# Kernel optimization log

Measured on AMD Instinct MI355X. Metric: run time of the kernel, lower is better.

## Reference

```python
import jax, jax.numpy as jnp
import numpy as np

WS = 8
NH = 6

def setup_inputs() -> dict:
    key = jax.random.key(0)
    ks = jax.random.split(key, 6)
    B, H, W, C = 4, 256, 256, 192
    return {
        "x": jax.random.normal(ks[0], (B, H * W, C), dtype=jnp.float32),
        "qkv_w": jax.random.normal(ks[1], (3 * C, C), dtype=jnp.float32) * 0.02,
        "qkv_b": jax.random.normal(ks[2], (3 * C,), dtype=jnp.float32) * 0.02,
        "proj_w": jax.random.normal(ks[3], (C, C), dtype=jnp.float32) * 0.02,
        "proj_b": jax.random.normal(ks[4], (C,), dtype=jnp.float32) * 0.02,
        "bias": jax.random.normal(ks[5], (NH, WS * WS, WS * WS), dtype=jnp.float32) * 0.02,
        "H": H,
        "W": W,
    }

def reference(x, qkv_w, qkv_b, proj_w, proj_b, bias, H, W):
    B, L, C = x.shape
    ws, nh = WS, NH
    hd = C // nh
    scale = hd ** -0.5
    H_pad = (H + ws - 1) // ws * ws
    W_pad = (W + ws - 1) // ws * ws
    pad_b, pad_r = H_pad - H, W_pad - W
    xv = x.reshape(B, H, W, C)
    if pad_b > 0 or pad_r > 0:
        xv = jnp.pad(xv, ((0, 0), (0, pad_b), (0, pad_r), (0, 0)))
    nHw, nWw = H_pad // ws, W_pad // ws
    # window partition: [B*nH*nW, ws*ws, C]
    xw = xv.reshape(B, nHw, ws, nWw, ws, C).transpose(0, 1, 3, 2, 4, 5)
    xw = xw.reshape(B * nHw * nWw, ws * ws, C)
    qkv = xw @ qkv_w.T + qkv_b  # [Bw, ws*ws, 3C]
    qkv = qkv.reshape(-1, ws * ws, 3, nh, hd).transpose(2, 0, 3, 1, 4)
    q, k, v = qkv[0], qkv[1], qkv[2]  # each [Bw, nh, ws*ws, hd]
    attn = jnp.einsum('bhqd,bhkd->bhqk', q * scale, k) + bias
    attn = jax.nn.softmax(attn, axis=-1)
    out = jnp.einsum('bhqk,bhkd->bhqd', attn, v)
    out = out.transpose(0, 2, 1, 3).reshape(-1, ws * ws, C)
    out = out @ proj_w.T + proj_b
    # window reverse: [B, H_pad, W_pad, C]
    out = out.reshape(B, nHw, nWw, ws, ws, C).transpose(0, 1, 3, 2, 4, 5)
    out = out.reshape(B, H_pad, W_pad, C)
    if pad_b > 0 or pad_r > 0:
        out = out[:, :H, :W, :]
    return out.reshape(B, H * W, C)
```

## Files before the change

kernel.cpp:

```cpp
#include <hip/hip_runtime.h>

typedef short bf16x8 __attribute__((ext_vector_type(8)));
typedef float f32x4 __attribute__((ext_vector_type(4)));

#define QKV_FRAG_SH 110592
#define PROJ_FRAG_SH 36864
#define BIAS2_OFF_B 294912
#define QKVB2_OFF_B 393216
#define SCALE 0.17677669529663689f
#define LOG2E 1.44269504088896341f
#define QSCALE (SCALE * LOG2E)
#define SMEM_BYTES 161792

__device__ __forceinline__ short f2bf(float f) {
  unsigned x = __float_as_uint(f);
  x = (x + 0x7FFFu + ((x >> 16) & 1u)) >> 16;
  return (short)x;
}

__global__ void cvt_w(const float* __restrict__ qkv_w,
                      const float* __restrict__ proj_w,
                      const float* __restrict__ bias,
                      const float* __restrict__ qkv_b,
                      short* __restrict__ wfrag,
                      float* __restrict__ bias2,
                      float* __restrict__ qkvb2) {
  int idx = blockIdx.x * 256 + threadIdx.x;
  if (idx < QKV_FRAG_SH) {
    int j = idx & 7, lane = (idx >> 3) & 63, t = idx >> 9;
    int nt = t / 6, ks = t - nt * 6;
    int n0 = nt * 16 + (lane & 15);
    float v = qkv_w[n0 * 192 + ks * 32 + (lane >> 4) * 8 + j];
    if (n0 < 192) v *= QSCALE;
    wfrag[idx] = f2bf(v);
  } else if (idx < QKV_FRAG_SH + PROJ_FRAG_SH) {
    int i2 = idx - QKV_FRAG_SH;
    int j = i2 & 7, lane = (i2 >> 3) & 63, t = i2 >> 9;
    int nt = t / 6, ks = t - nt * 6;
    wfrag[idx] = f2bf(proj_w[(nt * 16 + (lane & 15)) * 192 + ks * 32 + (lane >> 4) * 8 + j]);
  } else if (idx < QKV_FRAG_SH + PROJ_FRAG_SH + 24576) {
    int i3 = idx - (QKV_FRAG_SH + PROJ_FRAG_SH);
    int r = i3 & 3, nt = (i3 >> 2) & 3, lane = (i3 >> 4) & 63, mt = (i3 >> 10) & 3, h = i3 >> 12;
    int row = mt * 16 + (lane >> 4) * 4 + r;
    int col = nt * 16 + (lane & 15);
    bias2[i3] = bias[h * 4096 + row * 64 + col] * LOG2E;
  } else if (idx < QKV_FRAG_SH + PROJ_FRAG_SH + 24576 + 576) {
    int i4 = idx - (QKV_FRAG_SH + PROJ_FRAG_SH + 24576);
    qkvb2[i4] = qkv_b[i4] * (i4 < 192 ? QSCALE : 1.0f);
  }
}

__global__ __launch_bounds__(768, 3) void swin_fused(
    const float* __restrict__ x,
    const float* __restrict__ proj_b,
    const short* __restrict__ wfrag,
    const float* __restrict__ bias2,
    const float* __restrict__ qkvb2,
    float* __restrict__ out) {
  extern __shared__ short smem[];
  short* buf = smem;
  short* q_l = smem + 25600;
  short* k_l = smem + 39424;
  short* v_l = smem + 53248;
  short* p_s = smem + 67072;

  const short* wq = wfrag;
  const short* wp = wfrag + QKV_FRAG_SH;

  const int tid = threadIdx.x;
  const int w = tid >> 6, lane = tid & 63, quad = lane >> 4, lm = lane & 15;

  int goff[4], loff[4];
  #pragma unroll
  for (int i = 0; i < 4; ++i) {
    int idx4 = tid + i * 768;
    int chunk = idx4 / 384;
    int off = idx4 - chunk * 384;
    goff[i] = chunk * 49152 + off * 4;
    loff[i] = (chunk * 8 + off / 48) * 200 + (off % 48) * 4;
  }

  size_t base;
  {
    int wid = blockIdx.x;
    int b = wid >> 10, rem = wid & 1023, wh = rem >> 5, ww = rem & 31;
    base = ((size_t)b * 65536 + (size_t)(wh * 8) * 256 + (size_t)(ww * 8)) * 192;
    const float* xp = x + base;
    #pragma unroll
    for (int i = 0; i < 4; ++i) {
      float4 f = *(const float4*)(xp + goff[i]);
      short4 s = { f2bf(f.x), f2bf(f.y), f2bf(f.z), f2bf(f.w) };
      *(short4*)&buf[loff[i]] = s;
    }
  }
  __syncthreads();

  float4 pf[4];
  size_t nbase = 0;
  #pragma unroll 1
  for (int it = 0; it < 16; ++it) {
    const int cur = (it & 1) * 12800;
    const int nxt = 12800 - cur;

    if (it < 15) {
      int wid = (it + 1) * 256 + blockIdx.x;
      int b = wid >> 10, rem = wid & 1023, wh = rem >> 5, ww = rem & 31;
      nbase = ((size_t)b * 65536 + (size_t)(wh * 8) * 256 + (size_t)(ww * 8)) * 192;
      const float* xp = x + nbase;
      #pragma unroll
      for (int i = 0; i < 4; ++i) pf[i] = *(const float4*)(xp + goff[i]);
    }

    {
      const int nt0 = w * 3;
      f32x4 acc[3][4];
      #pragma unroll
      for (int j = 0; j < 3; ++j) {
        float bn = qkvb2[(nt0 + j) * 16 + lm];
        #pragma unroll
        for (int mm = 0; mm < 4; ++mm) acc[j][mm] = (f32x4){bn, bn, bn, bn};
      }
      #pragma unroll 2
      for (int ks = 0; ks < 6; ++ks) {
        bf16x8 a[4];
        #pragma unroll
        for (int mm = 0; mm < 4; ++mm)
          a[mm] = *(const bf16x8*)&buf[cur + (mm * 16 + lm) * 200 + ks * 32 + quad * 8];
        #pragma unroll
        for (int j = 0; j < 3; ++j) {
          bf16x8 bwf = *(const bf16x8*)&wq[((nt0 + j) * 6 + ks) * 512 + lane * 8];
          #pragma unroll
          for (int mm = 0; mm < 4; ++mm)
            acc[j][mm] = __builtin_amdgcn_mfma_f32_16x16x32_bf16(a[mm], bwf, acc[j][mm], 0, 0, 0);
        }
      }
      if (w < 4) {
        #pragma unroll
        for (int j = 0; j < 3; ++j) {
          int nt = nt0 + j, h = nt >> 1, dh = nt & 1;
          #pragma unroll
          for (int mm = 0; mm < 4; ++mm) {
            int rb = h * 64 + mm * 16 + quad * 4;
            #pragma unroll
            for (int r = 0; r < 4; ++r)
              q_l[(rb + r) * 36 + dh * 16 + lm] = f2bf(acc[j][mm][r]);
          }
        }
      } else if (w < 8) {
        #pragma unroll
        for (int j = 0; j < 3; ++j) {
          int nt = nt0 + j, h = (nt - 12) >> 1, dh = nt & 1;
          #pragma unroll
          for (int mm = 0; mm < 4; ++mm) {
            int rb = h * 64 + mm * 16 + quad * 4;
            #pragma unroll
            for (int r = 0; r < 4; ++r)
              k_l[(rb + r) * 36 + dh * 16 + lm] = f2bf(acc[j][mm][r]);
          }
        }
      } else {
        #pragma unroll
        for (int j = 0; j < 3; ++j) {
          int nt = nt0 + j, h = (nt - 24) >> 1, dh = nt & 1;
          #pragma unroll
          for (int mm = 0; mm < 4; ++mm) {
            short4 s4 = { f2bf(acc[j][mm][0]), f2bf(acc[j][mm][1]),
                          f2bf(acc[j][mm][2]), f2bf(acc[j][mm][3]) };
            *(short4*)&v_l[(h * 32 + dh * 16 + lm) * 72 + mm * 16 + quad * 4] = s4;
          }
        }
      }
    }
    __syncthreads();

    if (it < 15) {
      #pragma unroll
      for (int i = 0; i < 4; ++i) {
        short4 s = { f2bf(pf[i].x), f2bf(pf[i].y), f2bf(pf[i].z), f2bf(pf[i].w) };
        *(short4*)&buf[nxt + loff[i]] = s;
      }
    }

    {
      const int pb = w * 1152;
      #pragma unroll 1
      for (int i = 0; i < 2; ++i) {
        int tk = w + i * 12;
        int h = tk >> 2, mt = tk & 3;
        const float* bp = bias2 + ((h * 4 + mt) * 64 + lane) * 16;
        f32x4 lg[4];
        #pragma unroll
        for (int nt = 0; nt < 4; ++nt)
          lg[nt] = *(const f32x4*)(bp + nt * 4);
        bf16x8 aq = *(const bf16x8*)&q_l[(h * 64 + mt * 16 + lm) * 36 + quad * 8];
        #pragma unroll
        for (int nt = 0; nt < 4; ++nt) {
          bf16x8 bk = *(const bf16x8*)&k_l[(h * 64 + nt * 16 + lm) * 36 + quad * 8];
          lg[nt] = __builtin_amdgcn_mfma_f32_16x16x32_bf16(aq, bk, lg[nt], 0, 0, 0);
        }
        float s[4] = {0.f, 0.f, 0.f, 0.f};
        #pragma unroll
        for (int r = 0; r < 4; ++r) {
          #pragma unroll
          for (int nt = 0; nt < 4; ++nt) {
            float e = exp2f(lg[nt][r]);
            s[r] += e;
            p_s[pb + (quad * 4 + r) * 72 + nt * 16 + lm] = f2bf(e);
          }
        }
        #pragma unroll
        for (int r = 0; r < 4; ++r) {
          s[r] += __shfl_xor(s[r], 1);
          s[r] += __shfl_xor(s[r], 2);
          s[r] += __shfl_xor(s[r], 4);
          s[r] += __shfl_xor(s[r], 8);
        }
        asm volatile("s_waitcnt lgkmcnt(0)" ::: "memory");
        f32x4 o0 = {0.f,0.f,0.f,0.f}, o1 = {0.f,0.f,0.f,0.f};
        #pragma unroll
        for (int ks = 0; ks < 2; ++ks) {
          bf16x8 ap  = *(const bf16x8*)&p_s[pb + lm * 72 + ks * 32 + quad * 8];
          bf16x8 bv0 = *(const bf16x8*)&v_l[(h * 32 + lm) * 72 + ks * 32 + quad * 8];
          bf16x8 bv1 = *(const bf16x8*)&v_l[(h * 32 + 16 + lm) * 72 + ks * 32 + quad * 8];
          o0 = __builtin_amdgcn_mfma_f32_16x16x32_bf16(ap, bv0, o0, 0, 0, 0);
          o1 = __builtin_amdgcn_mfma_f32_16x16x32_bf16(ap, bv1, o1, 0, 0, 0);
        }
        #pragma unroll
        for (int r = 0; r < 4; ++r) {
          float ir = 1.0f / s[r];
          int rowo = cur + (mt * 16 + quad * 4 + r) * 200 + h * 32;
          buf[rowo + lm]      = f2bf(o0[r] * ir);
          buf[rowo + 16 + lm] = f2bf(o1[r] * ir);
        }
      }
    }
    __syncthreads();

    {
      const int nt = w;
      float pbv = proj_b[nt * 16 + lm];
      f32x4 acc[4];
      #pragma unroll
      for (int mm = 0; mm < 4; ++mm) acc[mm] = (f32x4){pbv, pbv, pbv, pbv};
      #pragma unroll 2
      for (int ks = 0; ks < 6; ++ks) {
        bf16x8 bwf = *(const bf16x8*)&wp[(nt * 6 + ks) * 512 + lane * 8];
        #pragma unroll
        for (int mm = 0; mm < 4; ++mm) {
          bf16x8 am = *(const bf16x8*)&buf[cur + (mm * 16 + lm) * 200 + ks * 32 + quad * 8];
          acc[mm] = __builtin_amdgcn_mfma_f32_16x16x32_bf16(am, bwf, acc[mm], 0, 0, 0);
        }
      }
      #pragma unroll
      for (int mm = 0; mm < 4; ++mm) {
        #pragma unroll
        for (int r = 0; r < 4; ++r) {
          int t = mm * 16 + quad * 4 + r;
          out[base + (size_t)((t >> 3) * 256 + (t & 7)) * 192 + nt * 16 + lm] = acc[mm][r];
        }
      }
    }
    base = nbase;
  }
}

extern "C" void kernel_launch(void* const* d_in, const int* in_sizes, int n_in,
                              void* d_out, int out_size, void* d_ws, size_t ws_size,
                              hipStream_t stream) {
  const float* x      = (const float*)d_in[0];
  const float* qkv_w  = (const float*)d_in[1];
  const float* qkv_b  = (const float*)d_in[2];
  const float* proj_w = (const float*)d_in[3];
  const float* proj_b = (const float*)d_in[4];
  const float* bias   = (const float*)d_in[5];
  short* wfrag = (short*)d_ws;
  float* bias2 = (float*)((char*)d_ws + BIAS2_OFF_B);
  float* qkvb2 = (float*)((char*)d_ws + QKVB2_OFF_B);

  hipFuncSetAttribute((const void*)swin_fused,
                      hipFuncAttributeMaxDynamicSharedMemorySize, SMEM_BYTES);

  hipLaunchKernelGGL(cvt_w, dim3(675), dim3(256), 0, stream,
                     qkv_w, proj_w, bias, qkv_b, wfrag, bias2, qkvb2);
  hipLaunchKernelGGL(swin_fused, dim3(256), dim3(768), SMEM_BYTES, stream,
                     x, proj_b, wfrag, bias2, qkvb2, (float*)d_out);
}
```

Measured before the change: 543.2 us.

## Keep QKV and proj weight fragments resident in registers across window iterations

Loads each wave's QKV and projection weight fragments (18 plus 6 bf16x8) and bias values into registers once, before the persistent 16-window loop, instead of re-reading them from global memory every iteration. The QKV GEMM is restructured to loop over row tiles with a small accumulator set, so the register budget can hold the weights. The attention bias tiles are prefetched before the barrier so their latency overlaps the sync. The cost is much higher VGPR pressure, which may reduce occupancy or cause spills.

New measurement: 586.2 us. 7.9% more time.

```diff
diff --git a/kernel.cpp b/kernel.cpp
--- a/kernel.cpp
+++ b/kernel.cpp
@@ -69,6 +69,23 @@
 
   const int tid = threadIdx.x;
   const int w = tid >> 6, lane = tid & 63, quad = lane >> 4, lm = lane & 15;
+  const int nt0 = w * 3;
+  const int mt = w & 3, hA = w >> 2;
+
+  bf16x8 wr[3][6];
+  #pragma unroll
+  for (int j = 0; j < 3; ++j)
+    #pragma unroll
+    for (int ks = 0; ks < 6; ++ks)
+      wr[j][ks] = *(const bf16x8*)&wq[((nt0 + j) * 6 + ks) * 512 + lane * 8];
+  bf16x8 wpf[6];
+  #pragma unroll
+  for (int ks = 0; ks < 6; ++ks)
+    wpf[ks] = *(const bf16x8*)&wp[(w * 6 + ks) * 512 + lane * 8];
+  float bn[3];
+  #pragma unroll
+  for (int j = 0; j < 3; ++j) bn[j] = qkvb2[(nt0 + j) * 16 + lm];
+  const float pbv = proj_b[w * 16 + lm];
 
   int goff[4], loff[4];
   #pragma unroll
@@ -112,64 +129,54 @@
     }
 
     {
-      const int nt0 = w * 3;
-      f32x4 acc[3][4];
-      #pragma unroll
-      for (int j = 0; j < 3; ++j) {
-        float bn = qkvb2[(nt0 + j) * 16 + lm];
-        #pragma unroll
-        for (int mm = 0; mm < 4; ++mm) acc[j][mm] = (f32x4){bn, bn, bn, bn};
-      }
-      #pragma unroll 2
-      for (int ks = 0; ks < 6; ++ks) {
-        bf16x8 a[4];
-        #pragma unroll
-        for (int mm = 0; mm < 4; ++mm)
-          a[mm] = *(const bf16x8*)&buf[cur + (mm * 16 + lm) * 200 + ks * 32 + quad * 8];
-        #pragma unroll
-        for (int j = 0; j < 3; ++j) {
-          bf16x8 bwf = *(const bf16x8*)&wq[((nt0 + j) * 6 + ks) * 512 + lane * 8];
-          #pragma unroll
-          for (int mm = 0; mm < 4; ++mm)
-            acc[j][mm] = __builtin_amdgcn_mfma_f32_16x16x32_bf16(a[mm], bwf, acc[j][mm], 0, 0, 0);
-        }
-      }
-      if (w < 4) {
-        #pragma unroll
-        for (int j = 0; j < 3; ++j) {
-          int nt = nt0 + j, h = nt >> 1, dh = nt & 1;
-          #pragma unroll
-          for (int mm = 0; mm < 4; ++mm) {
+      #pragma unroll 1
+      for (int mm = 0; mm < 4; ++mm) {
+        f32x4 acc[3];
+        #pragma unroll
+        for (int j = 0; j < 3; ++j) acc[j] = (f32x4){bn[j], bn[j], bn[j], bn[j]};
+        #pragma unroll
+        for (int ks = 0; ks < 6; ++ks) {
+          bf16x8 a = *(const bf16x8*)&buf[cur + (mm * 16 + lm) * 200 + ks * 32 + quad * 8];
+          #pragma unroll
+          for (int j = 0; j < 3; ++j)
+            acc[j] = __builtin_amdgcn_mfma_f32_16x16x32_bf16(a, wr[j][ks], acc[j], 0, 0, 0);
+        }
+        if (w < 4) {
+          #pragma unroll
+          for (int j = 0; j < 3; ++j) {
+            int nt = nt0 + j, h = nt >> 1, dh = nt & 1;
             int rb = h * 64 + mm * 16 + quad * 4;
             #pragma unroll
             for (int r = 0; r < 4; ++r)
-              q_l[(rb + r) * 36 + dh * 16 + lm] = f2bf(acc[j][mm][r]);
-          }
-        }
-      } else if (w < 8) {
-        #pragma unroll
-        for (int j = 0; j < 3; ++j) {
-          int nt = nt0 + j, h = (nt - 12) >> 1, dh = nt & 1;
-          #pragma unroll
-          for (int mm = 0; mm < 4; ++mm) {
+              q_l[(rb + r) * 36 + dh * 16 + lm] = f2bf(acc[j][r]);
+          }
+        } else if (w < 8) {
+          #pragma unroll
+          for (int j = 0; j < 3; ++j) {
+            int nt = nt0 + j, h = (nt - 12) >> 1, dh = nt & 1;
             int rb = h * 64 + mm * 16 + quad * 4;
             #pragma unroll
             for (int r = 0; r < 4; ++r)
-              k_l[(rb + r) * 36 + dh * 16 + lm] = f2bf(acc[j][mm][r]);
-          }
-        }
-      } else {
-        #pragma unroll
-        for (int j = 0; j < 3; ++j) {
-          int nt = nt0 + j, h = (nt - 24) >> 1, dh = nt & 1;
-          #pragma unroll
-          for (int mm = 0; mm < 4; ++mm) {
-            short4 s4 = { f2bf(acc[j][mm][0]), f2bf(acc[j][mm][1]),
-                          f2bf(acc[j][mm][2]), f2bf(acc[j][mm][3]) };
+              k_l[(rb + r) * 36 + dh * 16 + lm] = f2bf(acc[j][r]);
+          }
+        } else {
+          #pragma unroll
+          for (int j = 0; j < 3; ++j) {
+            int nt = nt0 + j, h = (nt - 24) >> 1, dh = nt & 1;
+            short4 s4 = { f2bf(acc[j][0]), f2bf(acc[j][1]),
+                          f2bf(acc[j][2]), f2bf(acc[j][3]) };
             *(short4*)&v_l[(h * 32 + dh * 16 + lm) * 72 + mm * 16 + quad * 4] = s4;
           }
         }
       }
+    }
+
+    f32x4 lgp[2][4];
+    #pragma unroll
+    for (int i = 0; i < 2; ++i) {
+      const float* bp = bias2 + (((hA + 3 * i) * 4 + mt) * 64 + lane) * 16;
+      #pragma unroll
+      for (int nt = 0; nt < 4; ++nt) lgp[i][nt] = *(const f32x4*)(bp + nt * 4);
     }
     __syncthreads();
 
@@ -183,27 +190,21 @@
 
     {
       const int pb = w * 1152;
-      #pragma unroll 1
+      #pragma unroll
       for (int i = 0; i < 2; ++i) {
-        int tk = w + i * 12;
-        int h = tk >> 2, mt = tk & 3;
-        const float* bp = bias2 + ((h * 4 + mt) * 64 + lane) * 16;
-        f32x4 lg[4];
-        #pragma unroll
-        for (int nt = 0; nt < 4; ++nt)
-          lg[nt] = *(const f32x4*)(bp + nt * 4);
+        const int h = hA + 3 * i;
         bf16x8 aq = *(const bf16x8*)&q_l[(h * 64 + mt * 16 + lm) * 36 + quad * 8];
         #pragma unroll
         for (int nt = 0; nt < 4; ++nt) {
           bf16x8 bk = *(const bf16x8*)&k_l[(h * 64 + nt * 16 + lm) * 36 + quad * 8];
-          lg[nt] = __builtin_amdgcn_mfma_f32_16x16x32_bf16(aq, bk, lg[nt], 0, 0, 0);
+          lgp[i][nt] = __builtin_amdgcn_mfma_f32_16x16x32_bf16(aq, bk, lgp[i][nt], 0, 0, 0);
         }
         float s[4] = {0.f, 0.f, 0.f, 0.f};
         #pragma unroll
         for (int r = 0; r < 4; ++r) {
           #pragma unroll
           for (int nt = 0; nt < 4; ++nt) {
-            float e = exp2f(lg[nt][r]);
+            float e = exp2f(lgp[i][nt][r]);
             s[r] += e;
             p_s[pb + (quad * 4 + r) * 72 + nt * 16 + lm] = f2bf(e);
           }
@@ -237,18 +238,15 @@
     __syncthreads();
 
     {
-      const int nt = w;
-      float pbv = proj_b[nt * 16 + lm];
       f32x4 acc[4];
       #pragma unroll
       for (int mm = 0; mm < 4; ++mm) acc[mm] = (f32x4){pbv, pbv, pbv, pbv};
-      #pragma unroll 2
+      #pragma unroll
       for (int ks = 0; ks < 6; ++ks) {
-        bf16x8 bwf = *(const bf16x8*)&wp[(nt * 6 + ks) * 512 + lane * 8];
         #pragma unroll
         for (int mm = 0; mm < 4; ++mm) {
           bf16x8 am = *(const bf16x8*)&buf[cur + (mm * 16 + lm) * 200 + ks * 32 + quad * 8];
-          acc[mm] = __builtin_amdgcn_mfma_f32_16x16x32_bf16(am, bwf, acc[mm], 0, 0, 0);
+          acc[mm] = __builtin_amdgcn_mfma_f32_16x16x32_bf16(am, wpf[ks], acc[mm], 0, 0, 0);
         }
       }
       #pragma unroll
@@ -256,7 +254,7 @@
         #pragma unroll
         for (int r = 0; r < 4; ++r) {
           int t = mm * 16 + quad * 4 + r;
-          out[base + (size_t)((t >> 3) * 256 + (t & 7)) * 192 + nt * 16 + lm] = acc[mm][r];
+          out[base + (size_t)((t >> 3) * 256 + (t & 7)) * 192 + w * 16 + lm] = acc[mm][r];
         }
       }
     }
```
